# Kernel tuning notes

Hardware: AMD Instinct MI355X
Metric: run time of the kernel (lower is better)

Reference implementation:

```python
import jax, jax.numpy as jnp
import numpy as np

B, F, D = 2048, 40, 32
CIN = (64, 64)


def _glorot(key, shape):
    fan_in, fan_out = shape[1] * shape[2], shape[0] * shape[2]
    std = jnp.sqrt(2.0 / (fan_in + fan_out)).astype(jnp.float32)
    return jax.random.normal(key, shape, dtype=jnp.float32) * std


def setup_inputs() -> dict:
    key = jax.random.key(0)
    kx, k0, k1 = jax.random.split(key, 3)
    x = jax.random.normal(kx, (B, F, D), dtype=jnp.float32)
    W0 = _glorot(k0, (CIN[0], F * F, D))
    b0 = jnp.zeros((CIN[0],), dtype=jnp.float32)
    W1 = _glorot(k1, (CIN[1], F * CIN[0], D))
    b1 = jnp.zeros((CIN[1],), dtype=jnp.float32)
    return {"x": x, "W0": W0, "b0": b0, "W1": W1, "b1": b1}


def _cin_step(x0, xk, W, b):
    # x0: (B,F,D)  xk: (B,H,D)  W: (O, H*F, D)  b: (O,)
    Bn, H, Dn = xk.shape
    Fn = x0.shape[1]
    # outer product per embedding channel, h-major flatten as in tf.reshape
    z = jnp.einsum('bhd,bfd->bhfd', xk, x0).reshape(Bn, H * Fn, Dn)
    # per-embedding-channel contraction against weights: (B,D,O)
    y = jnp.einsum('bhd,ohd->bdo', z, W) + b
    y = jax.nn.relu(y)
    return jnp.transpose(y, (0, 2, 1))  # (B,O,D)


def reference(x, W0, b0, W1, b1):
    x1 = _cin_step(x, x, W0, b0)
    x2 = _cin_step(x, x1, W1, b1)
    final = jnp.concatenate([x, x1, x2], axis=1)  # (B, F+O0+O1, D)
    return jnp.sum(final, axis=-1)  # (B, F+O0+O1)
```

## Files before the change

### kernel.cpp

```cpp
#include <hip/hip_runtime.h>

typedef unsigned int   u32;
typedef unsigned short u16;
typedef _Float16       f16;

using f16x8  = __attribute__((ext_vector_type(8)))  _Float16;
using f16x4  = __attribute__((ext_vector_type(4)))  _Float16;
using f32x16 = __attribute__((ext_vector_type(16))) float;

#define LLDS16(G, L) __builtin_amdgcn_global_load_lds( \
  (const __attribute__((address_space(1))) u32*)(G), \
  (__attribute__((address_space(3))) u32*)(L), 16, 0, 0)

#define WAITV(N) { asm volatile("s_waitcnt vmcnt(" #N ")" ::: "memory"); \
                   __builtin_amdgcn_sched_barrier(0); }
#define FENCE_BAR() { asm volatile("s_waitcnt lgkmcnt(0)" ::: "memory"); \
                      __builtin_amdgcn_sched_barrier(0); \
                      __builtin_amdgcn_s_barrier(); \
                      __builtin_amdgcn_sched_barrier(0); }
#define BAR() { __builtin_amdgcn_s_barrier(); __builtin_amdgcn_sched_barrier(0); }
#define KEEP(x) asm volatile("" : "+v"(x))

__global__ __launch_bounds__(256)
void prep(const float* __restrict__ x,
          const float* __restrict__ W0, const float* __restrict__ W1,
          f16* __restrict__ xt, f16* __restrict__ W0p, f16* __restrict__ W1p,
          float* __restrict__ out){
  __shared__ char shm[33920];
  const int tid = threadIdx.x;
  if (blockIdx.x < 2560){
    float (*tile)[33] = (float(*)[33])shm;
    const int r0 = blockIdx.x << 5;
    const int c  = tid & 31;
    const int rp = tid >> 5;
#pragma unroll
    for (int p = 0; p < 4; ++p){
      const int r = (p << 3) + rp;
      float v = x[(size_t)(r0 + r) * 32 + c];
      tile[r][c] = v;
      float s = v;
#pragma unroll
      for (int off = 16; off > 0; off >>= 1) s += __shfl_xor(s, off, 32);
      if (c == 0){
        const int row = r0 + r;
        out[(size_t)(row / 40) * 168 + (row % 40)] = s;
      }
    }
    __syncthreads();
#pragma unroll
    for (int p = 0; p < 4; ++p){
      const int dd = (p << 3) + rp;
      xt[(size_t)dd * 81920 + r0 + c] = (f16)tile[c][dd];
    }
  } else {
    u16* t = (u16*)shm;
    int kb = blockIdx.x - 2560;
    const float* in; f16* outp; int K;
    if (kb < 200){ in = W0; outp = W0p; K = 1600; }
    else         { kb -= 200; in = W1; outp = W1p; K = 2560; }
    const int kbase = kb << 3;
#pragma unroll 4
    for (int i = 0; i < 64; ++i){
      const int idx = tid + (i << 8);
      const int o   = idx >> 8;
      const int rem = idx & 255;
      const int e   = rem >> 5;
      const int dd  = rem & 31;
      const float v = in[(size_t)o * (K * 32) + (size_t)(kbase + e) * 32 + dd];
      union { f16 h; u16 u; } cv; cv.h = (f16)v;
      t[dd * 530 + o * 8 + e] = cv.u;
    }
    __syncthreads();
    const u32* t32 = (const u32*)t;
    u32* o32 = (u32*)outp;
    const int obase = kb << 8;
#pragma unroll 4
    for (int i = 0; i < 32; ++i){
      const int idx = tid + (i << 8);
      const int dd  = idx >> 8;
      const int rem = idx & 255;
      o32[(size_t)dd * (K * 32) + obase + rem] = t32[dd * 265 + rem];
    }
  }
}

__global__ __launch_bounds__(256, 2)
void cin_fused(const f16* __restrict__ xt,
               const f16* __restrict__ W0p,
               const f16* __restrict__ W1p,
               const float* __restrict__ b0v, const float* __restrict__ b1v,
               f16* __restrict__ x1s,
               f16* __restrict__ y2s){
  constexpr int XOFF = 61440;
  constexpr int X0MS = 32 * 96;
  constexpr int X1MS = 32 * 144;

  const int bid = blockIdx.x;
  const int d   = ((bid & 7) << 2) | ((bid >> 3) & 3);
  const int b0  = (bid >> 5) << 7;
  const int tid = threadIdx.x;
  const int wv  = tid >> 6;
  const int wr  = wv >> 1;
  const int wc  = wv & 1;
  const int l   = tid & 63;
  const int hi  = l >> 5;
  const int lr  = l & 31;

  __shared__ char smem[79872];

  const f16* gW0 = W0p + (size_t)d * 102400;
  const f16* gW1 = W1p + (size_t)d * 163840;

#define ISSUE(I, BUF) do { \
    const f16* src_ = ((I) < 10) ? (gW0 + (size_t)(I) * 10240) \
                                 : (gW1 + (size_t)((I) - 10) * 10240); \
    const f16* gt_ = src_ + l * 8; \
    char* lb_ = smem + (BUF) * 20480; \
    _Pragma("unroll") \
    for (int j_ = 0; j_ < 5; ++j_) \
      LLDS16(gt_ + (size_t)(wv + 4 * j_) * 512, lb_ + (wv + 4 * j_) * 1024); \
  } while (0)

  ISSUE(0, 0);
  ISSUE(1, 1);

  {
    const uint4* src = (const uint4*)(xt + (size_t)d * 81920 + (size_t)b0 * 40);
#pragma unroll
    for (int it = 0; it < 3; ++it){
      const int idx = tid + (it << 8);
      if (idx < 640){
        const int r = idx / 5, c = idx - r * 5;
        *(uint4*)(smem + XOFF + r * 96 + c * 16) = src[idx];
      }
    }
  }
  __syncthreads();

  const char* x0r = smem + XOFF + ((wr << 6) + lr) * 96;
  const char* x1r = smem + XOFF + ((wr << 6) + lr) * 144;
  const int   col = (wc << 5) + lr;
  const float bv1 = b0v[col];
  const float bv2 = b1v[col];

  f16x8 sl[2][5];
#pragma unroll
  for (int m = 0; m < 2; ++m){
    const char* xe = x0r + m * X0MS + hi * 16;
#pragma unroll
    for (int t = 0; t < 4; ++t) sl[m][t] = *(const f16x8*)(xe + t * 16);
    sl[m][4] = *(const f16x8*)(x0r + m * X0MS + (hi ? 0 : 64));
  }
  KEEP(sl[0][0]); KEEP(sl[0][1]); KEEP(sl[0][2]); KEEP(sl[0][3]); KEEP(sl[0][4]);
  KEEP(sl[1][0]); KEEP(sl[1][1]); KEEP(sl[1][2]); KEEP(sl[1][3]); KEEP(sl[1][4]);

  const f32x16 fz = {0,0,0,0,0,0,0,0,0,0,0,0,0,0,0,0};
  f32x16 acc0a = fz, acc0b = fz, acc1a = fz, acc1b = fz;

  const int vb = (hi << 10) + (wc << 9) + (lr << 4);

  static constexpr int J0[5]  = {0, 4, 3, 2, 1};
  static constexpr int H0[5]  = {0, 0, 1, 2, 3};
  static constexpr int H0b[5] = {0, 1, 1, 2, 3};
  static constexpr int S0[5]  = {0, 1, 0, 0, 0};
  static constexpr int J2[5]  = {2, 1, 0, 4, 3};
  static constexpr int H2[5]  = {0, 1, 2, 2, 3};
  static constexpr int H2b[5] = {0, 1, 2, 3, 3};
  static constexpr int S2[5]  = {0, 0, 0, 1, 0};

#define COMP(BB) do { \
  __builtin_amdgcn_s_setprio(1); \
  _Pragma("unroll") \
  for (int si = 0; si < 5; ++si){ \
    const f16x8 bf0 = *(const f16x8*)((BB) + vb + si * 4096); \
    const f16x8 bf2 = *(const f16x8*)((BB) + vb + si * 4096 + 2048); \
    const f16 xa00 = (S0[si] && hi) ? xh0[H0b[si]] : xh0[H0[si]]; \
    const f16 xa01 = (S0[si] && hi) ? xh1[H0b[si]] : xh1[H0[si]]; \
    const f16 xa20 = (S2[si] && hi) ? xh0[H2b[si]] : xh0[H2[si]]; \
    const f16 xa21 = (S2[si] && hi) ? xh1[H2b[si]] : xh1[H2[si]]; \
    acc0a = __builtin_amdgcn_mfma_f32_32x32x16_f16(sl[0][J0[si]] * xa00, bf0, acc0a, 0, 0, 0); \
    acc1a = __builtin_amdgcn_mfma_f32_32x32x16_f16(sl[1][J0[si]] * xa01, bf0, acc1a, 0, 0, 0); \
    acc0b = __builtin_amdgcn_mfma_f32_32x32x16_f16(sl[0][J2[si]] * xa20, bf2, acc0b, 0, 0, 0); \
    acc1b = __builtin_amdgcn_mfma_f32_32x32x16_f16(sl[1][J2[si]] * xa21, bf2, acc1b, 0, 0, 0); \
  } \
  __builtin_amdgcn_s_setprio(0); \
} while (0)

  int cur = 0, ib = 2;

  for (int t = 0; t < 10; ++t){
    if (t > 0){ WAITV(5); BAR(); }
    ISSUE(t + 2, ib);
    const f16x4 xh0 = *(const f16x4*)(x0r + t * 8);
    const f16x4 xh1 = *(const f16x4*)(x0r + X0MS + t * 8);
    COMP(smem + cur * 20480);
    cur = cur + 1; if (cur == 3) cur = 0;
    ib  = ib + 1;  if (ib == 3)  ib = 0;
  }

  {
    FENCE_BAR();
    u16* x1w = (u16*)(smem + XOFF);
#pragma unroll
    for (int m = 0; m < 2; ++m)
#pragma unroll
      for (int reg = 0; reg < 16; ++reg){
        const int row = (wr << 6) + (m << 5) + (reg & 3) + ((reg >> 2) << 3) + (hi << 2);
        float v = (m ? acc1a[reg] + acc1b[reg] : acc0a[reg] + acc0b[reg]) + bv1;
        v = v > 0.f ? v : 0.f;
        union { f16 h; u16 u; } cv; cv.h = (f16)v;
        x1w[row * 72 + col] = cv.u;
      }
    acc0a = fz; acc0b = fz; acc1a = fz; acc1b = fz;
    FENCE_BAR();
#pragma unroll
    for (int it = 0; it < 4; ++it){
      const int u   = tid + (it << 8);
      const int row = u >> 3, ch = u & 7;
      const f16x8 vv = *(const f16x8*)((const char*)x1w + row * 144 + ch * 16);
      *(f16x8*)(x1s + (size_t)(b0 + row) * 2048 + d * 64 + ch * 8) = vv;
    }
  }

  for (int t2 = 0; t2 < 16; ++t2){
    if (t2 < 2)       { WAITV(9); }
    else if (t2 < 15) { WAITV(5); }
    else              { WAITV(0); }
    BAR();
    if (t2 + 2 < 16) ISSUE(12 + t2, ib);
    const f16x4 xh0 = *(const f16x4*)(x1r + t2 * 8);
    const f16x4 xh1 = *(const f16x4*)(x1r + X1MS + t2 * 8);
    COMP(smem + cur * 20480);
    cur = cur + 1; if (cur == 3) cur = 0;
    ib  = ib + 1;  if (ib == 3)  ib = 0;
  }

  {
    FENCE_BAR();
    u16* yw = (u16*)(smem + XOFF);
#pragma unroll
    for (int m = 0; m < 2; ++m)
#pragma unroll
      for (int reg = 0; reg < 16; ++reg){
        const int row = (wr << 6) + (m << 5) + (reg & 3) + ((reg >> 2) << 3) + (hi << 2);
        float v = (m ? acc1a[reg] + acc1b[reg] : acc0a[reg] + acc0b[reg]) + bv2;
        v = v > 0.f ? v : 0.f;
        union { f16 h; u16 u; } cv; cv.h = (f16)v;
        yw[row * 72 + col] = cv.u;
      }
    FENCE_BAR();
#pragma unroll
    for (int it = 0; it < 4; ++it){
      const int u   = tid + (it << 8);
      const int row = u >> 3, ch = u & 7;
      const f16x8 vv = *(const f16x8*)((const char*)yw + row * 144 + ch * 16);
      *(f16x8*)(y2s + (size_t)(b0 + row) * 2048 + d * 64 + ch * 8) = vv;
    }
  }
#undef ISSUE
#undef COMP
}

__global__ __launch_bounds__(128)
void finalize(const f16* __restrict__ x1s, const f16* __restrict__ y2s,
              float* __restrict__ out){
  const int b = blockIdx.x;
  const int t = threadIdx.x;
  if (t < 64){
    float s = 0.f;
#pragma unroll
    for (int d = 0; d < 32; ++d) s += (float)x1s[(size_t)b * 2048 + d * 64 + t];
    out[(size_t)b * 168 + 40 + t] = s;
  } else {
    const int o = t - 64;
    float s = 0.f;
#pragma unroll
    for (int d = 0; d < 32; ++d) s += (float)y2s[(size_t)b * 2048 + d * 64 + o];
    out[(size_t)b * 168 + 104 + o] = s;
  }
}

extern "C" void kernel_launch(void* const* d_in, const int* in_sizes, int n_in,
                              void* d_out, int out_size, void* d_ws, size_t ws_size,
                              hipStream_t stream){
  const float* x   = (const float*)d_in[0];
  const float* W0  = (const float*)d_in[1];
  const float* b0v = (const float*)d_in[2];
  const float* W1  = (const float*)d_in[3];
  const float* b1v = (const float*)d_in[4];
  float* out = (float*)d_out;

  char* ws = (char*)d_ws;
  f16* xt  = (f16*)(ws + 0);
  f16* W0p = (f16*)(ws + 5242880);
  f16* W1p = (f16*)(ws + 11796480);
  f16* x1s = (f16*)(ws + 22282240);
  f16* y2s = (f16*)(ws + 30670848);

  prep<<<3080, 256, 0, stream>>>(x, W0, W1, xt, W0p, W1p, out);
  cin_fused<<<512, 256, 0, stream>>>(xt, W0p, W1p, b0v, b1v, x1s, y2s);
  finalize<<<2048, 128, 0, stream>>>(x1s, y2s, out);
}
```

Before: 60.43 us.

## Split K across waves, load weights directly to registers, halve batch tile

The fused CIN kernel now uses 64-row batch tiles and launches twice as many blocks. Each pair of waves splits the K (h) dimension in half, and the partial accumulators are combined through LDS before the bias and ReLU. Weight fragments are loaded straight from global memory into registers with double buffering, replacing the LDS staging ring and its vmcnt/barrier choreography. This cuts LDS use and raises parallelism, at the cost of redundant global weight reads per block, exposed global load latency, and an extra reduction step.

```diff
diff --git a/kernel.cpp b/kernel.cpp
--- a/kernel.cpp
+++ b/kernel.cpp
@@ -5,20 +5,9 @@
 typedef _Float16       f16;
 
 using f16x8  = __attribute__((ext_vector_type(8)))  _Float16;
-using f16x4  = __attribute__((ext_vector_type(4)))  _Float16;
+using f16x2  = __attribute__((ext_vector_type(2)))  _Float16;
 using f32x16 = __attribute__((ext_vector_type(16))) float;
 
-#define LLDS16(G, L) __builtin_amdgcn_global_load_lds( \
-  (const __attribute__((address_space(1))) u32*)(G), \
-  (__attribute__((address_space(3))) u32*)(L), 16, 0, 0)
-
-#define WAITV(N) { asm volatile("s_waitcnt vmcnt(" #N ")" ::: "memory"); \
-                   __builtin_amdgcn_sched_barrier(0); }
-#define FENCE_BAR() { asm volatile("s_waitcnt lgkmcnt(0)" ::: "memory"); \
-                      __builtin_amdgcn_sched_barrier(0); \
-                      __builtin_amdgcn_s_barrier(); \
-                      __builtin_amdgcn_sched_barrier(0); }
-#define BAR() { __builtin_amdgcn_s_barrier(); __builtin_amdgcn_sched_barrier(0); }
 #define KEEP(x) asm volatile("" : "+v"(x))
 
 __global__ __launch_bounds__(256)
@@ -91,45 +80,43 @@
                const float* __restrict__ b0v, const float* __restrict__ b1v,
                f16* __restrict__ x1s,
                f16* __restrict__ y2s){
-  constexpr int XOFF = 61440;
-  constexpr int X0MS = 32 * 96;
-  constexpr int X1MS = 32 * 144;
+  constexpr int XOFF = 16896;
 
   const int bid = blockIdx.x;
   const int d   = ((bid & 7) << 2) | ((bid >> 3) & 3);
-  const int b0  = (bid >> 5) << 7;
+  const int b0  = (bid >> 5) << 6;
   const int tid = threadIdx.x;
   const int wv  = tid >> 6;
-  const int wr  = wv >> 1;
+  const int kh  = wv >> 1;
   const int wc  = wv & 1;
   const int l   = tid & 63;
   const int hi  = l >> 5;
   const int lr  = l & 31;
 
-  __shared__ char smem[79872];
+  __shared__ char smem[26112];
 
   const f16* gW0 = W0p + (size_t)d * 102400;
   const f16* gW1 = W1p + (size_t)d * 163840;
-
-#define ISSUE(I, BUF) do { \
-    const f16* src_ = ((I) < 10) ? (gW0 + (size_t)(I) * 10240) \
-                                 : (gW1 + (size_t)((I) - 10) * 10240); \
-    const f16* gt_ = src_ + l * 8; \
-    char* lb_ = smem + (BUF) * 20480; \
+  const int lane_off = hi * 512 + ((wc << 5) + lr) * 8;
+
+  f16x8 B0[5], B1[5];
+
+#define LOADB(B, GP, TT) do { \
     _Pragma("unroll") \
-    for (int j_ = 0; j_ < 5; ++j_) \
-      LLDS16(gt_ + (size_t)(wv + 4 * j_) * 512, lb_ + (wv + 4 * j_) * 1024); \
+    for (int mi_ = 0; mi_ < 5; ++mi_) \
+      (B)[mi_] = *(const f16x8*)((GP) + (size_t)(TT) * 5120 + mi_ * 1024); \
+    __builtin_amdgcn_sched_barrier(0); \
   } while (0)
 
-  ISSUE(0, 0);
-  ISSUE(1, 1);
+  const f16* g1 = gW0 + kh * 51200 + lane_off;
+  LOADB(B0, g1, 0);
 
   {
     const uint4* src = (const uint4*)(xt + (size_t)d * 81920 + (size_t)b0 * 40);
 #pragma unroll
-    for (int it = 0; it < 3; ++it){
+    for (int it = 0; it < 2; ++it){
       const int idx = tid + (it << 8);
-      if (idx < 640){
+      if (idx < 320){
         const int r = idx / 5, c = idx - r * 5;
         *(uint4*)(smem + XOFF + r * 96 + c * 16) = src[idx];
       }
@@ -137,8 +124,8 @@
   }
   __syncthreads();
 
-  const char* x0r = smem + XOFF + ((wr << 6) + lr) * 96;
-  const char* x1r = smem + XOFF + ((wr << 6) + lr) * 144;
+  const char* x0row = smem + XOFF + lr * 96;
+  const char* x1row = smem + XOFF + lr * 144;
   const int   col = (wc << 5) + lr;
   const float bv1 = b0v[col];
   const float bv2 = b1v[col];
@@ -146,75 +133,76 @@
   f16x8 sl[2][5];
 #pragma unroll
   for (int m = 0; m < 2; ++m){
-    const char* xe = x0r + m * X0MS + hi * 16;
+    const char* xe = x0row + m * 3072 + hi * 16;
 #pragma unroll
     for (int t = 0; t < 4; ++t) sl[m][t] = *(const f16x8*)(xe + t * 16);
-    sl[m][4] = *(const f16x8*)(x0r + m * X0MS + (hi ? 0 : 64));
+    sl[m][4] = *(const f16x8*)(x0row + m * 3072 + (hi ? 0 : 64));
   }
   KEEP(sl[0][0]); KEEP(sl[0][1]); KEEP(sl[0][2]); KEEP(sl[0][3]); KEEP(sl[0][4]);
   KEEP(sl[1][0]); KEEP(sl[1][1]); KEEP(sl[1][2]); KEEP(sl[1][3]); KEEP(sl[1][4]);
 
   const f32x16 fz = {0,0,0,0,0,0,0,0,0,0,0,0,0,0,0,0};
-  f32x16 acc0a = fz, acc0b = fz, acc1a = fz, acc1b = fz;
-
-  const int vb = (hi << 10) + (wc << 9) + (lr << 4);
-
-  static constexpr int J0[5]  = {0, 4, 3, 2, 1};
-  static constexpr int H0[5]  = {0, 0, 1, 2, 3};
-  static constexpr int H0b[5] = {0, 1, 1, 2, 3};
-  static constexpr int S0[5]  = {0, 1, 0, 0, 0};
-  static constexpr int J2[5]  = {2, 1, 0, 4, 3};
-  static constexpr int H2[5]  = {0, 1, 2, 2, 3};
-  static constexpr int H2b[5] = {0, 1, 2, 3, 3};
-  static constexpr int S2[5]  = {0, 0, 0, 1, 0};
-
-#define COMP(BB) do { \
-  __builtin_amdgcn_s_setprio(1); \
-  _Pragma("unroll") \
-  for (int si = 0; si < 5; ++si){ \
-    const f16x8 bf0 = *(const f16x8*)((BB) + vb + si * 4096); \
-    const f16x8 bf2 = *(const f16x8*)((BB) + vb + si * 4096 + 2048); \
-    const f16 xa00 = (S0[si] && hi) ? xh0[H0b[si]] : xh0[H0[si]]; \
-    const f16 xa01 = (S0[si] && hi) ? xh1[H0b[si]] : xh1[H0[si]]; \
-    const f16 xa20 = (S2[si] && hi) ? xh0[H2b[si]] : xh0[H2[si]]; \
-    const f16 xa21 = (S2[si] && hi) ? xh1[H2b[si]] : xh1[H2[si]]; \
-    acc0a = __builtin_amdgcn_mfma_f32_32x32x16_f16(sl[0][J0[si]] * xa00, bf0, acc0a, 0, 0, 0); \
-    acc1a = __builtin_amdgcn_mfma_f32_32x32x16_f16(sl[1][J0[si]] * xa01, bf0, acc1a, 0, 0, 0); \
-    acc0b = __builtin_amdgcn_mfma_f32_32x32x16_f16(sl[0][J2[si]] * xa20, bf2, acc0b, 0, 0, 0); \
-    acc1b = __builtin_amdgcn_mfma_f32_32x32x16_f16(sl[1][J2[si]] * xa21, bf2, acc1b, 0, 0, 0); \
-  } \
-  __builtin_amdgcn_s_setprio(0); \
-} while (0)
-
-  int cur = 0, ib = 2;
-
-  for (int t = 0; t < 10; ++t){
-    if (t > 0){ WAITV(5); BAR(); }
-    ISSUE(t + 2, ib);
-    const f16x4 xh0 = *(const f16x4*)(x0r + t * 8);
-    const f16x4 xh1 = *(const f16x4*)(x0r + X0MS + t * 8);
-    COMP(smem + cur * 20480);
-    cur = cur + 1; if (cur == 3) cur = 0;
-    ib  = ib + 1;  if (ib == 3)  ib = 0;
-  }
-
-  {
-    FENCE_BAR();
-    u16* x1w = (u16*)(smem + XOFF);
-#pragma unroll
-    for (int m = 0; m < 2; ++m)
-#pragma unroll
-      for (int reg = 0; reg < 16; ++reg){
-        const int row = (wr << 6) + (m << 5) + (reg & 3) + ((reg >> 2) << 3) + (hi << 2);
-        float v = (m ? acc1a[reg] + acc1b[reg] : acc0a[reg] + acc0b[reg]) + bv1;
+  f32x16 accA = fz, accB = fz;
+
+  static constexpr int SI[5] = {0, 2, 4, 1, 3};
+
+#define COMP(B, XB, TT, HOFF, MS) do { \
+    const f16x2 xhp0 = *(const f16x2*)((XB) + (HOFF) + (TT) * 4); \
+    const f16x2 xhp1 = *(const f16x2*)((XB) + (HOFF) + (TT) * 4 + (MS)); \
+    __builtin_amdgcn_s_setprio(1); \
+    _Pragma("unroll") \
+    for (int mi = 0; mi < 5; ++mi){ \
+      const f16x8 bf = (B)[mi]; \
+      const f16 xa0 = (mi < 2) ? xhp0[0] : (mi > 2) ? xhp0[1] : (hi ? xhp0[1] : xhp0[0]); \
+      const f16 xa1 = (mi < 2) ? xhp1[0] : (mi > 2) ? xhp1[1] : (hi ? xhp1[1] : xhp1[0]); \
+      accA = __builtin_amdgcn_mfma_f32_32x32x16_f16(sl[0][SI[mi]] * xa0, bf, accA, 0, 0, 0); \
+      accB = __builtin_amdgcn_mfma_f32_32x32x16_f16(sl[1][SI[mi]] * xa1, bf, accB, 0, 0, 0); \
+    } \
+    __builtin_amdgcn_s_setprio(0); \
+  } while (0)
+
+  {
+    const int hoff = kh * 40;
+    for (int t = 0; t < 10; t += 2){
+      LOADB(B1, g1, t + 1);
+      COMP(B0, x0row, t, hoff, 3072);
+      LOADB(B0, g1, t + 2);
+      COMP(B1, x0row, t + 1, hoff, 3072);
+    }
+  }
+
+  float* redp = (float*)(smem + wc * 8448);
+  u16*   x1w  = (u16*)(smem + XOFF);
+  if (kh == 1){
+#pragma unroll
+    for (int m = 0; m < 2; ++m)
+#pragma unroll
+      for (int reg = 0; reg < 16; ++reg){
+        const int row = (m << 5) + (reg & 3) + ((reg >> 2) << 3) + (hi << 2);
+        redp[row * 33 + lr] = (m ? accB[reg] : accA[reg]);
+      }
+  }
+  __syncthreads();
+  if (kh == 0){
+#pragma unroll
+    for (int m = 0; m < 2; ++m)
+#pragma unroll
+      for (int reg = 0; reg < 16; ++reg){
+        const int row = (m << 5) + (reg & 3) + ((reg >> 2) << 3) + (hi << 2);
+        float v = (m ? accB[reg] : accA[reg]) + redp[row * 33 + lr] + bv1;
         v = v > 0.f ? v : 0.f;
         union { f16 h; u16 u; } cv; cv.h = (f16)v;
         x1w[row * 72 + col] = cv.u;
       }
-    acc0a = fz; acc0b = fz; acc1a = fz; acc1b = fz;
-    FENCE_BAR();
-#pragma unroll
-    for (int it = 0; it < 4; ++it){
+  }
+  accA = fz; accB = fz;
+  const f16* g2 = gW1 + kh * 81920 + lane_off;
+  LOADB(B0, g2, 0);
+  __syncthreads();
+
+  {
+#pragma unroll
+    for (int it = 0; it < 2; ++it){
       const int u   = tid + (it << 8);
       const int row = u >> 3, ch = u & 7;
       const f16x8 vv = *(const f16x8*)((const char*)x1w + row * 144 + ch * 16);
@@ -222,42 +210,49 @@
     }
   }
 
-  for (int t2 = 0; t2 < 16; ++t2){
-    if (t2 < 2)       { WAITV(9); }
-    else if (t2 < 15) { WAITV(5); }
-    else              { WAITV(0); }
-    BAR();
-    if (t2 + 2 < 16) ISSUE(12 + t2, ib);
-    const f16x4 xh0 = *(const f16x4*)(x1r + t2 * 8);
-    const f16x4 xh1 = *(const f16x4*)(x1r + X1MS + t2 * 8);
-    COMP(smem + cur * 20480);
-    cur = cur + 1; if (cur == 3) cur = 0;
-    ib  = ib + 1;  if (ib == 3)  ib = 0;
-  }
-
-  {
-    FENCE_BAR();
-    u16* yw = (u16*)(smem + XOFF);
-#pragma unroll
-    for (int m = 0; m < 2; ++m)
-#pragma unroll
-      for (int reg = 0; reg < 16; ++reg){
-        const int row = (wr << 6) + (m << 5) + (reg & 3) + ((reg >> 2) << 3) + (hi << 2);
-        float v = (m ? acc1a[reg] + acc1b[reg] : acc0a[reg] + acc0b[reg]) + bv2;
+  {
+    const int hoff = kh * 64;
+    for (int t = 0; t < 16; t += 2){
+      LOADB(B1, g2, t + 1);
+      COMP(B0, x1row, t, hoff, 4608);
+      LOADB(B0, g2, t + 2);
+      COMP(B1, x1row, t + 1, hoff, 4608);
+    }
+  }
+
+  if (kh == 1){
+#pragma unroll
+    for (int m = 0; m < 2; ++m)
+#pragma unroll
+      for (int reg = 0; reg < 16; ++reg){
+        const int row = (m << 5) + (reg & 3) + ((reg >> 2) << 3) + (hi << 2);
+        redp[row * 33 + lr] = (m ? accB[reg] : accA[reg]);
+      }
+  }
+  __syncthreads();
+  if (kh == 0){
+#pragma unroll
+    for (int m = 0; m < 2; ++m)
+#pragma unroll
+      for (int reg = 0; reg < 16; ++reg){
+        const int row = (m << 5) + (reg & 3) + ((reg >> 2) << 3) + (hi << 2);
+        float v = (m ? accB[reg] : accA[reg]) + redp[row * 33 + lr] + bv2;
         v = v > 0.f ? v : 0.f;
         union { f16 h; u16 u; } cv; cv.h = (f16)v;
-        yw[row * 72 + col] = cv.u;
-      }
-    FENCE_BAR();
-#pragma unroll
-    for (int it = 0; it < 4; ++it){
+        x1w[row * 72 + col] = cv.u;
+      }
+  }
+  __syncthreads();
+  {
+#pragma unroll
+    for (int it = 0; it < 2; ++it){
       const int u   = tid + (it << 8);
       const int row = u >> 3, ch = u & 7;
-      const f16x8 vv = *(const f16x8*)((const char*)yw + row * 144 + ch * 16);
+      const f16x8 vv = *(const f16x8*)((const char*)x1w + row * 144 + ch * 16);
       *(f16x8*)(y2s + (size_t)(b0 + row) * 2048 + d * 64 + ch * 8) = vv;
     }
   }
-#undef ISSUE
+#undef LOADB
 #undef COMP
 }
 
@@ -298,6 +293,6 @@
   f16* y2s = (f16*)(ws + 30670848);
 
   prep<<<3080, 256, 0, stream>>>(x, W0, W1, xt, W0p, W1p, out);
-  cin_fused<<<512, 256, 0, stream>>>(xt, W0p, W1p, b0v, b1v, x1s, y2s);
+  cin_fused<<<1024, 256, 0, stream>>>(xt, W0p, W1p, b0v, b1v, x1s, y2s);
   finalize<<<2048, 128, 0, stream>>>(x1s, y2s, out);
 }
```

Measured after the change: 62.87 us. 4.0% more time.
